# Kernel optimization log

Hardware: AMD Instinct MI355X
Metric: run time of the kernel (lower is better)

The kernel has to match this reference:

```python
import jax, jax.numpy as jnp
import numpy as np

BN_EPS = 1e-5


def conv_bn_relu(x, w, b, gamma, beta):
    # Conv2d(stride=2, padding=1) -> BatchNorm2d (training-mode batch stats) -> ReLU
    y = jax.lax.conv_general_dilated(
        x, w, window_strides=(2, 2), padding=((1, 1), (1, 1)),
        dimension_numbers=('NCHW', 'OIHW', 'NCHW')) + b[None, :, None, None]
    mu = y.mean(axis=(0, 2, 3))
    var = y.var(axis=(0, 2, 3))
    y = (y - mu[None, :, None, None]) * jax.lax.rsqrt(var + BN_EPS)[None, :, None, None]
    y = y * gamma[None, :, None, None] + beta[None, :, None, None]
    return jax.nn.relu(y)


def setup_inputs() -> dict:
    key = jax.random.key(0)
    ks = jax.random.split(key, 12)
    N, C, HW_IN = 32, 3, 64
    SD = 24           # stem_dim
    RQ = 128          # rnn_hidden_dim
    MD = 128          # module_dim
    FC = 1024         # classifier hidden
    NA = 2            # num answers
    D_PAIR = (SD + 2) * 2 + RQ  # 180
    s = 0.05
    return {
        'image':   jax.random.normal(ks[0], (N, C, HW_IN, HW_IN), jnp.float32),
        'ques':    jax.random.normal(ks[1], (N, RQ), jnp.float32),
        'conv1_w': jax.random.normal(ks[2], (SD, C, 3, 3), jnp.float32) * s,
        'conv1_b': jnp.zeros((SD,), jnp.float32),
        'bn1_g':   jnp.ones((SD,), jnp.float32),
        'bn1_b':   jnp.zeros((SD,), jnp.float32),
        'conv2_w': jax.random.normal(ks[3], (SD, SD, 3, 3), jnp.float32) * s,
        'conv2_b': jnp.zeros((SD,), jnp.float32),
        'bn2_g':   jnp.ones((SD,), jnp.float32),
        'bn2_b':   jnp.zeros((SD,), jnp.float32),
        'w_rel':   jax.random.normal(ks[4], (D_PAIR, MD), jnp.float32) * s,
        'b_rel':   jnp.zeros((MD,), jnp.float32),
        'w_fc1':   jax.random.normal(ks[5], (MD, FC), jnp.float32) * s,
        'b_fc1':   jnp.zeros((FC,), jnp.float32),
        'w_fc2':   jax.random.normal(ks[6], (FC, NA), jnp.float32) * s,
        'b_fc2':   jnp.zeros((NA,), jnp.float32),
    }


def reference(image, ques, conv1_w, conv1_b, bn1_g, bn1_b,
              conv2_w, conv2_b, bn2_g, bn2_b,
              w_rel, b_rel, w_fc1, b_fc1, w_fc2, b_fc2):
    f = conv_bn_relu(image, conv1_w, conv1_b, bn1_g, bn1_b)
    f = conv_bn_relu(f, conv2_w, conv2_b, bn2_g, bn2_b)
    N, F, H, W = f.shape
    HW = H * W
    flat = f.reshape(N, F, HW).transpose(0, 2, 1)      # (N, HW, F)

    # coordinate grid exactly as in the torch code (stacked over (W, H))
    xs = jnp.linspace(-1.0, 1.0, W)
    ys = jnp.linspace(-1.0, 1.0, H)
    xv = jnp.repeat(xs[:, None], H, axis=1)            # (W, H)
    yv = jnp.repeat(ys[None, :], W, axis=0)            # (W, H)
    coords = jnp.stack([xv, yv], axis=2).reshape(-1, 2)  # (HW, 2)

    fc = jnp.concatenate(
        [flat, jnp.broadcast_to(coords[None], (N, HW, 2))], axis=2)  # (N, HW, F+2)
    D = F + 2

    # relation layer is a single Linear over cat([x_i, x_j, ques]) followed by
    # a sum over ALL (HW)^2 pairs. Because the layer is linear, the pair sum
    # decomposes exactly:
    #   sum_{a,b} (fc[b] Wi + fc[a] Wj + q Wq + b_rel)
    # = HW * (sum_p fc[p]) (Wi + Wj) + HW^2 * (q Wq + b_rel)
    Wi, Wj, Wq = w_rel[:D], w_rel[D:2 * D], w_rel[2 * D:]
    s = fc.sum(axis=1)                                  # (N, D)
    hw = jnp.asarray(HW, fc.dtype)
    relations = hw * (s @ (Wi + Wj)) + (hw * hw) * (ques @ Wq + b_rel)  # (N, 128)

    # ---- classifier: Linear -> ReLU -> Linear ----
    h = jax.nn.relu(relations @ w_fc1 + b_fc1)
    out = h @ w_fc2 + b_fc2                             # (N, num_answers)
    return out
```

## Files before the change

### kernel.cpp

```cpp
#include <hip/hip_runtime.h>
#include <math.h>


#define N_BATCH 32
#define C_OUT 24
#define NBLK 192
#define MAGIC 0x13579BDFu
#define AGENT __HIP_MEMORY_SCOPE_AGENT
#define PITCH 40
#define NROWS 33
#define CHSZ (PITCH * NROWS)

__device__ __forceinline__ float aload(const float* p) {
  return __hip_atomic_load(p, __ATOMIC_RELAXED, AGENT);
}
__device__ __forceinline__ void astore(float* p, float v) {
  __hip_atomic_store(p, v, __ATOMIC_RELAXED, AGENT);
}
__device__ __forceinline__ void waitflag(const unsigned* f) {
  while (__hip_atomic_load(f, __ATOMIC_RELAXED, AGENT) != MAGIC)
    __builtin_amdgcn_s_sleep(1);
}

__global__ __launch_bounds__(1024) void fused_kernel(
    const float* __restrict__ img, const float* __restrict__ ques,
    const float* __restrict__ c1w, const float* __restrict__ c1b,
    const float* __restrict__ g1,  const float* __restrict__ bt1,
    const float* __restrict__ c2w, const float* __restrict__ c2b,
    const float* __restrict__ g2,  const float* __restrict__ bt2,
    const float* __restrict__ w_rel, const float* __restrict__ b_rel,
    const float* __restrict__ w_fc1, const float* __restrict__ b_fc1,
    const float* __restrict__ w_fc2, const float* __restrict__ b_fc2,
    float* __restrict__ out,
    unsigned* __restrict__ flags1, unsigned* __restrict__ flags2,
    unsigned* __restrict__ flags3,
    float* __restrict__ p1, float* __restrict__ p2,
    float* __restrict__ ssum) {
  const int t = threadIdx.x;
  const int bid = blockIdx.x;
  const int lane = t & 63, wid = t >> 6;
  const int n = bid & 31;
  const int r = bid >> 5;

  __shared__ unsigned short y1u[24 * CHSZ];
  __shared__ float red[5120];
  __shared__ float s_a[C_OUT], s_b[C_OUT];
  __shared__ float a2[4], b2[4];
  __shared__ float chS[16], chS2[16];
  __shared__ float qpart[1024];
  __shared__ float qfull[128];
  __shared__ float s_s[26];
  __shared__ float s_coef[128];
  __shared__ float s_h[1024];

  if (t < 24 * PITCH) {
    int ch = t / PITCH;
    y1u[ch * CHSZ + (t - ch * PITCH)] = 0;
  }
  if (t < 768)
    y1u[(t >> 5) * CHSZ + ((t & 31) + 1) * PITCH] = 0;

  {
    int oh = t >> 5, ow = t & 31;
    float win[27];
    #pragma unroll
    for (int ci = 0; ci < 3; ci++)
      #pragma unroll
      for (int kh = 0; kh < 3; kh++) {
        int ih = oh * 2 - 1 + kh;
        #pragma unroll
        for (int kw = 0; kw < 3; kw++) {
          int iw = ow * 2 - 1 + kw;
          win[ci * 9 + kh * 3 + kw] =
              (ih >= 0 && iw >= 0) ? img[(n * 3 + ci) * 4096 + ih * 64 + iw] : 0.f;
        }
      }
    #pragma unroll
    for (int co = 0; co < C_OUT; co++) {
      float acc = c1b[co];
      #pragma unroll
      for (int q = 0; q < 27; q++) acc += win[q] * c1w[co * 27 + q];
      unsigned bits = __float_as_uint(acc);
      unsigned rr = (bits + 0x7FFFu + ((bits >> 16) & 1u)) >> 16;
      y1u[co * CHSZ + (oh + 1) * PITCH + (ow + 1)] = (unsigned short)rr;
    }
  }
  __syncthreads();

  if (r == 0) {
    if (t < 768) {
      int ch = t >> 5, l = t & 31;
      float s = 0.f, s2 = 0.f;
      #pragma unroll
      for (int i = 0; i < 32; i++) {
        float x = __uint_as_float(
            (unsigned)y1u[ch * CHSZ + (i + 1) * PITCH + (l + 1)] << 16);
        s += x; s2 += x * x;
      }
      #pragma unroll
      for (int off = 16; off > 0; off >>= 1) {
        s += __shfl_down(s, off, 32);
        s2 += __shfl_down(s2, off, 32);
      }
      if (l == 0) {
        astore(&p1[ch * 32 + n], s);
        astore(&p1[768 + ch * 32 + n], s2);
      }
    }
    __syncthreads();
    if (t == 0)
      __hip_atomic_store(&flags1[n], MAGIC, __ATOMIC_RELEASE, AGENT);
  }

  if (t < 32) waitflag(&flags1[t]);
  __syncthreads();
  if (t < 768) {
    int ch = t >> 5, j = t & 31;
    float s = aload(&p1[ch * 32 + j]);
    float s2 = aload(&p1[768 + ch * 32 + j]);
    #pragma unroll
    for (int off = 16; off > 0; off >>= 1) {
      s += __shfl_down(s, off, 32);
      s2 += __shfl_down(s2, off, 32);
    }
    if (j == 0) {
      float mu = s * (1.f / 32768.f);
      float var = s2 * (1.f / 32768.f) - mu * mu;
      float a = rsqrtf(var + 1e-5f) * g1[ch];
      s_a[ch] = a;
      s_b[ch] = bt1[ch] - mu * a;
    }
  }
  __syncthreads();

  const int px = t & 255;
  const int slot = t >> 8;
  const int co2 = r * 4 + slot;
  float acc2;
  {
    const int o2h = px >> 4, o2w = px & 15;
    float accq[4] = {0.f, 0.f, 0.f, 0.f};
    const int ci0 = slot * 6;
    #pragma unroll
    for (int cc = 0; cc < 6; cc++) {
      const int ci = ci0 + cc;
      const float a1 = s_a[ci], b1 = s_b[ci];
      const unsigned* chp = (const unsigned*)(y1u + ci * CHSZ);
      #pragma unroll
      for (int kh = 0; kh < 3; kh++) {
        const int row = o2h * 2 + kh;
        const unsigned* pr = chp + row * (PITCH / 2);
        unsigned w0 = pr[o2w];
        unsigned w1 = pr[o2w + 1];
        float x0 = __uint_as_float(w0 << 16);
        float x1 = __uint_as_float(w0 & 0xffff0000u);
        float x2 = __uint_as_float(w1 << 16);
        x0 = fmaxf(fmaf(x0, a1, b1), 0.f);
        x1 = fmaxf(fmaf(x1, a1, b1), 0.f);
        x2 = fmaxf(fmaf(x2, a1, b1), 0.f);
        if (row == 0) { x0 = 0.f; x1 = 0.f; x2 = 0.f; }
        if (o2w == 0) x0 = 0.f;
        #pragma unroll
        for (int co = 0; co < 4; co++) {
          const float* wp = c2w + ((r * 4 + co) * C_OUT + ci) * 9 + kh * 3;
          accq[co] = fmaf(x0, wp[0], accq[co]);
          accq[co] = fmaf(x1, wp[1], accq[co]);
          accq[co] = fmaf(x2, wp[2], accq[co]);
        }
      }
    }
    #pragma unroll
    for (int q = 0; q < 4; q++) red[(slot * 256 + px) * 5 + q] = accq[q];
  }
  __syncthreads();
  {
    acc2 = c2b[co2];
    #pragma unroll
    for (int s = 0; s < 4; s++) acc2 += red[(s * 256 + px) * 5 + slot];
  }
  {
    float s = acc2, s2 = acc2 * acc2;
    #pragma unroll
    for (int off = 32; off > 0; off >>= 1) {
      s += __shfl_down(s, off, 64);
      s2 += __shfl_down(s2, off, 64);
    }
    if (lane == 0) { chS[slot * 4 + (wid & 3)] = s; chS2[slot * 4 + (wid & 3)] = s2; }
  }
  __syncthreads();
  if (t < 4) {
    float s = chS[t * 4] + chS[t * 4 + 1] + chS[t * 4 + 2] + chS[t * 4 + 3];
    float s2 = chS2[t * 4] + chS2[t * 4 + 1] + chS2[t * 4 + 2] + chS2[t * 4 + 3];
    astore(&p2[(r * 4 + t) * 32 + n], s);
    astore(&p2[768 + (r * 4 + t) * 32 + n], s2);
  }
  __syncthreads();
  if (t == 0)
    __hip_atomic_store(&flags2[bid], MAGIC, __ATOMIC_RELEASE, AGENT);

  if (r == 0) {
    {
      float pf = 0.f;
      #pragma unroll
      for (int i = 0; i < 4; i++) pf += w_fc1[(t + i * 1024) * 32];
      if (t < 208) pf += w_rel[t * 32];
      if (t < 64)  pf += w_fc2[t * 32];
      if (t < 32)  pf += b_fc1[t * 32];
      asm volatile("" :: "v"(pf));
    }
    {
      int m = t & 127, g = t >> 7;
      const float* qv = ques + n * 128;
      float q = 0.f;
      for (int k = g * 16; k < g * 16 + 16; k++)
        q += qv[k] * w_rel[(52 + k) * 128 + m];
      qpart[t] = q;
    }
    __syncthreads();
    if (t < 128) {
      float q = b_rel[t];
      #pragma unroll
      for (int g = 0; g < 8; g++) q += qpart[g * 128 + t];
      qfull[t] = 65536.f * q;
    }
  }

  if (t < 32) waitflag(&flags2[r * 32 + t]);
  __syncthreads();
  if (t < 128) {
    int c4 = t >> 5, j = t & 31;
    float s = aload(&p2[(r * 4 + c4) * 32 + j]);
    float s2 = aload(&p2[768 + (r * 4 + c4) * 32 + j]);
    #pragma unroll
    for (int off = 16; off > 0; off >>= 1) {
      s += __shfl_down(s, off, 32);
      s2 += __shfl_down(s2, off, 32);
    }
    if (j == 0) {
      float mu = s * (1.f / 8192.f);
      float var = s2 * (1.f / 8192.f) - mu * mu;
      float a = rsqrtf(var + 1e-5f) * g2[r * 4 + c4];
      a2[c4] = a;
      b2[c4] = bt2[r * 4 + c4] - mu * a;
    }
  }
  __syncthreads();

  {
    float v = acc2 * a2[slot] + b2[slot];
    v = v > 0.f ? v : 0.f;
    #pragma unroll
    for (int off = 32; off > 0; off >>= 1) v += __shfl_down(v, off, 64);
    if (lane == 0) chS[slot * 4 + (wid & 3)] = v;
  }
  __syncthreads();
  if (t < 4)
    astore(&ssum[n * C_OUT + r * 4 + t],
           chS[t * 4] + chS[t * 4 + 1] + chS[t * 4 + 2] + chS[t * 4 + 3]);
  __syncthreads();
  if (t == 0)
    __hip_atomic_store(&flags3[bid], MAGIC, __ATOMIC_RELEASE, AGENT);

  if (r != 0) return;

  if (t >= 1 && t < 6) waitflag(&flags3[t * 32 + n]);
  __syncthreads();
  if (t < C_OUT) s_s[t] = aload(&ssum[n * C_OUT + t]);
  if (t == 24 || t == 25) {
    float cs = 0.f;
    for (int i = 0; i < 16; i++) cs += -1.f + 2.f * (float)i / 15.f;
    s_s[t] = 16.f * cs;
  }
  __syncthreads();

  {
    int col = t & 127, g = t >> 7;
    float p = 0.f;
    #pragma unroll
    for (int dd = 0; dd < 4; dd++) {
      int d = g + dd * 8;
      if (d < 26)
        p += s_s[d] * (w_rel[d * 128 + col] + w_rel[(26 + d) * 128 + col]);
    }
    qpart[t] = p;
  }
  __syncthreads();
  if (t < 128) {
    float sterm = 0.f;
    #pragma unroll
    for (int g = 0; g < 8; g++) sterm += qpart[g * 128 + t];
    s_coef[t] = qfull[t] + 256.f * sterm;
  }
  __syncthreads();

  {
    const int cg = t & 255, mg = t >> 8;
    const float4* wp = (const float4*)(w_fc1) + mg * 32 * 256 + cg;
    float4 acc = make_float4(0.f, 0.f, 0.f, 0.f);
    #pragma unroll 8
    for (int k = 0; k < 32; k++) {
      float c = s_coef[mg * 32 + k];
      float4 w = wp[k * 256];
      acc.x += c * w.x; acc.y += c * w.y; acc.z += c * w.z; acc.w += c * w.w;
    }
    red[cg * 17 + mg * 4 + 0] = acc.x;
    red[cg * 17 + mg * 4 + 1] = acc.y;
    red[cg * 17 + mg * 4 + 2] = acc.z;
    red[cg * 17 + mg * 4 + 3] = acc.w;
  }
  __syncthreads();
  {
    float h = b_fc1[t];
    #pragma unroll
    for (int mg = 0; mg < 4; mg++) h += red[(t >> 2) * 17 + mg * 4 + (t & 3)];
    s_h[t] = h > 0.f ? h : 0.f;
  }
  __syncthreads();

  {
    float hv = s_h[t];
    float a0 = hv * w_fc2[2 * t], a1 = hv * w_fc2[2 * t + 1];
    #pragma unroll
    for (int off = 32; off > 0; off >>= 1) {
      a0 += __shfl_down(a0, off, 64);
      a1 += __shfl_down(a1, off, 64);
    }
    if (lane == 0) { chS[wid] = a0; chS2[wid] = a1; }
  }
  __syncthreads();
  if (t == 0) {
    float a0 = 0.f, a1 = 0.f;
    #pragma unroll
    for (int i = 0; i < 16; i++) { a0 += chS[i]; a1 += chS2[i]; }
    out[n * 2 + 0] = a0 + b_fc2[0];
    out[n * 2 + 1] = a1 + b_fc2[1];
  }
}

extern "C" void kernel_launch(void* const* d_in, const int* in_sizes, int n_in,
                              void* d_out, int out_size, void* d_ws, size_t ws_size,
                              hipStream_t stream) {
  const float* image   = (const float*)d_in[0];
  const float* ques    = (const float*)d_in[1];
  const float* conv1_w = (const float*)d_in[2];
  const float* conv1_b = (const float*)d_in[3];
  const float* bn1_g   = (const float*)d_in[4];
  const float* bn1_b   = (const float*)d_in[5];
  const float* conv2_w = (const float*)d_in[6];
  const float* conv2_b = (const float*)d_in[7];
  const float* bn2_g   = (const float*)d_in[8];
  const float* bn2_b   = (const float*)d_in[9];
  const float* w_rel   = (const float*)d_in[10];
  const float* b_rel   = (const float*)d_in[11];
  const float* w_fc1   = (const float*)d_in[12];
  const float* b_fc1   = (const float*)d_in[13];
  const float* w_fc2   = (const float*)d_in[14];
  const float* b_fc2   = (const float*)d_in[15];
  float* out = (float*)d_out;

  unsigned* flags1 = (unsigned*)d_ws;
  unsigned* flags2 = flags1 + 32;
  unsigned* flags3 = flags2 + 192;
  float* p1   = (float*)d_ws + 416;
  float* p2   = p1 + 1536;
  float* ssum = p2 + 1536;

  fused_kernel<<<NBLK, 1024, 0, stream>>>(
      image, ques, conv1_w, conv1_b, bn1_g, bn1_b, conv2_w, conv2_b,
      bn2_g, bn2_b, w_rel, b_rel, w_fc1, b_fc1, w_fc2, b_fc2,
      out, flags1, flags2, flags3, p1, p2, ssum);
}
```

Measured before the change: 120.7 us.

## Split classifier FC1/FC2 across all six row-blocks per sample

Before, only the r==0 block of each sample computed the 128x1024 FC1 and FC2 tail while the other five blocks exited. Now every block computes the relation coefficients and its own slice of about 43 float4 column groups of FC1. It reduces FC2 partials for that slice and hands them to r==0 through a new flag and partial buffer. Weight prefetch is also spread across all blocks earlier. This cuts the serial tail on one block per sample, at the cost of an extra cross-block handoff and redundant qfull/coef computation in every block.

```diff
diff --git a/kernel.cpp b/kernel.cpp
--- a/kernel.cpp
+++ b/kernel.cpp
@@ -33,17 +33,20 @@
     const float* __restrict__ w_fc2, const float* __restrict__ b_fc2,
     float* __restrict__ out,
     unsigned* __restrict__ flags1, unsigned* __restrict__ flags2,
-    unsigned* __restrict__ flags3,
+    unsigned* __restrict__ flags3, unsigned* __restrict__ flags4,
     float* __restrict__ p1, float* __restrict__ p2,
-    float* __restrict__ ssum) {
+    float* __restrict__ ssum, float* __restrict__ pairs) {
   const int t = threadIdx.x;
   const int bid = blockIdx.x;
   const int lane = t & 63, wid = t >> 6;
   const int n = bid & 31;
   const int r = bid >> 5;
 
+  const int g0 = r * 43 - (r == 5 ? 1 : 0);
+  const int gcnt = (r < 4) ? 43 : 42;
+
   __shared__ unsigned short y1u[24 * CHSZ];
-  __shared__ float red[5120];
+  __align__(16) __shared__ float red[5120];
   __shared__ float s_a[C_OUT], s_b[C_OUT];
   __shared__ float a2[4], b2[4];
   __shared__ float chS[16], chS2[16];
@@ -51,7 +54,6 @@
   __shared__ float qfull[128];
   __shared__ float s_s[26];
   __shared__ float s_coef[128];
-  __shared__ float s_h[1024];
 
   if (t < 24 * PITCH) {
     int ch = t / PITCH;
@@ -110,6 +112,20 @@
     __syncthreads();
     if (t == 0)
       __hip_atomic_store(&flags1[n], MAGIC, __ATOMIC_RELEASE, AGENT);
+  }
+
+  {
+    float pf = 0.f;
+    {
+      int row = t >> 3, l = t & 7;
+      int col = g0 * 4 + l * 32;
+      col = col < 1024 ? col : 1023;
+      pf += w_fc1[row * 1024 + col];
+    }
+    if (t < 720) pf += w_rel[t * 32];
+    if (t < 64)  pf += w_fc2[t * 32];
+    if (t < 32)  pf += b_fc1[t * 32];
+    asm volatile("" :: "v"(pf));
   }
 
   if (t < 32) waitflag(&flags1[t]);
@@ -198,31 +214,20 @@
   if (t == 0)
     __hip_atomic_store(&flags2[bid], MAGIC, __ATOMIC_RELEASE, AGENT);
 
-  if (r == 0) {
-    {
-      float pf = 0.f;
-      #pragma unroll
-      for (int i = 0; i < 4; i++) pf += w_fc1[(t + i * 1024) * 32];
-      if (t < 208) pf += w_rel[t * 32];
-      if (t < 64)  pf += w_fc2[t * 32];
-      if (t < 32)  pf += b_fc1[t * 32];
-      asm volatile("" :: "v"(pf));
-    }
-    {
-      int m = t & 127, g = t >> 7;
-      const float* qv = ques + n * 128;
-      float q = 0.f;
-      for (int k = g * 16; k < g * 16 + 16; k++)
-        q += qv[k] * w_rel[(52 + k) * 128 + m];
-      qpart[t] = q;
-    }
-    __syncthreads();
-    if (t < 128) {
-      float q = b_rel[t];
-      #pragma unroll
-      for (int g = 0; g < 8; g++) q += qpart[g * 128 + t];
-      qfull[t] = 65536.f * q;
-    }
+  {
+    int m = t & 127, g = t >> 7;
+    const float* qv = ques + n * 128;
+    float q = 0.f;
+    for (int k = g * 16; k < g * 16 + 16; k++)
+      q += qv[k] * w_rel[(52 + k) * 128 + m];
+    qpart[t] = q;
+  }
+  __syncthreads();
+  if (t < 128) {
+    float q = b_rel[t];
+    #pragma unroll
+    for (int g = 0; g < 8; g++) q += qpart[g * 128 + t];
+    qfull[t] = 65536.f * q;
   }
 
   if (t < 32) waitflag(&flags2[r * 32 + t]);
@@ -261,9 +266,7 @@
   if (t == 0)
     __hip_atomic_store(&flags3[bid], MAGIC, __ATOMIC_RELEASE, AGENT);
 
-  if (r != 0) return;
-
-  if (t >= 1 && t < 6) waitflag(&flags3[t * 32 + n]);
+  if (t < 6 && t != r) waitflag(&flags3[t * 32 + n]);
   __syncthreads();
   if (t < C_OUT) s_s[t] = aload(&ssum[n * C_OUT + t]);
   if (t == 24 || t == 25) {
@@ -294,32 +297,33 @@
   __syncthreads();
 
   {
-    const int cg = t & 255, mg = t >> 8;
-    const float4* wp = (const float4*)(w_fc1) + mg * 32 * 256 + cg;
-    float4 acc = make_float4(0.f, 0.f, 0.f, 0.f);
-    #pragma unroll 8
-    for (int k = 0; k < 32; k++) {
-      float c = s_coef[mg * 32 + k];
-      float4 w = wp[k * 256];
-      acc.x += c * w.x; acc.y += c * w.y; acc.z += c * w.z; acc.w += c * w.w;
-    }
-    red[cg * 17 + mg * 4 + 0] = acc.x;
-    red[cg * 17 + mg * 4 + 1] = acc.y;
-    red[cg * 17 + mg * 4 + 2] = acc.z;
-    red[cg * 17 + mg * 4 + 3] = acc.w;
-  }
-  __syncthreads();
-  {
-    float h = b_fc1[t];
-    #pragma unroll
-    for (int mg = 0; mg < 4; mg++) h += red[(t >> 2) * 17 + mg * 4 + (t & 3)];
-    s_h[t] = h > 0.f ? h : 0.f;
-  }
-  __syncthreads();
-
-  {
-    float hv = s_h[t];
-    float a0 = hv * w_fc2[2 * t], a1 = hv * w_fc2[2 * t + 1];
+    const int gi = lane, mseg = wid;
+    if (gi < gcnt) {
+      const float4* wp = (const float4*)w_fc1 + (g0 + gi);
+      float4 acc = make_float4(0.f, 0.f, 0.f, 0.f);
+      #pragma unroll
+      for (int k = 0; k < 8; k++) {
+        int m = mseg * 8 + k;
+        float c = s_coef[m];
+        float4 w = wp[m * 256];
+        acc.x += c * w.x; acc.y += c * w.y; acc.z += c * w.z; acc.w += c * w.w;
+      }
+      ((float4*)red)[mseg * 43 + gi] = acc;
+    }
+  }
+  __syncthreads();
+  float a0 = 0.f, a1 = 0.f;
+  if (t < gcnt * 4) {
+    const int gcol = g0 * 4 + t;
+    float h = b_fc1[gcol];
+    #pragma unroll
+    for (int mseg = 0; mseg < 16; mseg++) h += red[mseg * 172 + t];
+    h = h > 0.f ? h : 0.f;
+    a0 = h * w_fc2[2 * gcol];
+    a1 = h * w_fc2[2 * gcol + 1];
+  }
+  __syncthreads();
+  {
     #pragma unroll
     for (int off = 32; off > 0; off >>= 1) {
       a0 += __shfl_down(a0, off, 64);
@@ -329,11 +333,30 @@
   }
   __syncthreads();
   if (t == 0) {
-    float a0 = 0.f, a1 = 0.f;
-    #pragma unroll
-    for (int i = 0; i < 16; i++) { a0 += chS[i]; a1 += chS2[i]; }
-    out[n * 2 + 0] = a0 + b_fc2[0];
-    out[n * 2 + 1] = a1 + b_fc2[1];
+    float b0 = 0.f, b1v = 0.f;
+    #pragma unroll
+    for (int i = 0; i < 16; i++) { b0 += chS[i]; b1v += chS2[i]; }
+    if (r != 0) {
+      astore(&pairs[n * 12 + r * 2 + 0], b0);
+      astore(&pairs[n * 12 + r * 2 + 1], b1v);
+      __hip_atomic_store(&flags4[bid], MAGIC, __ATOMIC_RELEASE, AGENT);
+    } else {
+      chS[0] = b0; chS2[0] = b1v;
+    }
+  }
+  if (r != 0) return;
+
+  if (t >= 1 && t < 6) waitflag(&flags4[t * 32 + n]);
+  __syncthreads();
+  if (t == 0) {
+    float b0 = chS[0], b1v = chS2[0];
+    #pragma unroll
+    for (int i = 1; i < 6; i++) {
+      b0 += aload(&pairs[n * 12 + i * 2 + 0]);
+      b1v += aload(&pairs[n * 12 + i * 2 + 1]);
+    }
+    out[n * 2 + 0] = b0 + b_fc2[0];
+    out[n * 2 + 1] = b1v + b_fc2[1];
   }
 }
 
@@ -361,12 +384,14 @@
   unsigned* flags1 = (unsigned*)d_ws;
   unsigned* flags2 = flags1 + 32;
   unsigned* flags3 = flags2 + 192;
-  float* p1   = (float*)d_ws + 416;
-  float* p2   = p1 + 1536;
-  float* ssum = p2 + 1536;
+  unsigned* flags4 = flags3 + 192;
+  float* p1    = (float*)d_ws + 608;
+  float* p2    = p1 + 1536;
+  float* ssum  = p2 + 1536;
+  float* pairs = ssum + 768;
 
   fused_kernel<<<NBLK, 1024, 0, stream>>>(
       image, ques, conv1_w, conv1_b, bn1_g, bn1_b, conv2_w, conv2_b,
       bn2_g, bn2_b, w_rel, b_rel, w_fc1, b_fc1, w_fc2, b_fc2,
-      out, flags1, flags2, flags3, p1, p2, ssum);
-}
+      out, flags1, flags2, flags3, flags4, p1, p2, ssum, pairs);
+}
```

Result: slower. 124.4 us (+3.0%).

## Collapse to one block per image, dropping cross-block output-channel split and third barrier

Applied to the files above, without the earlier changes.

Launches 32 blocks (one per batch image) instead of 192, so each block computes all 24 conv2 output channels itself rather than splitting channels across 6 blocks. This removes the in-block partial-sum reduction through shared memory, the third global flag barrier and the ssum exchange. It also reuses the y1 shared buffer for the FC reduction and widens the L2 prefetch of w_rel. The cost is that conv2 work per block grows sixfold and only 32 CUs are used, so the critical path per block lengthens.

```diff
diff --git a/kernel.cpp b/kernel.cpp
--- a/kernel.cpp
+++ b/kernel.cpp
@@ -2,14 +2,12 @@
 #include <math.h>
 
 
-#define N_BATCH 32
-#define C_OUT 24
-#define NBLK 192
 #define MAGIC 0x13579BDFu
 #define AGENT __HIP_MEMORY_SCOPE_AGENT
 #define PITCH 40
 #define NROWS 33
 #define CHSZ (PITCH * NROWS)
+#define C_OUT 24
 
 __device__ __forceinline__ float aload(const float* p) {
   return __hip_atomic_load(p, __ATOMIC_RELAXED, AGENT);
@@ -33,25 +31,21 @@
     const float* __restrict__ w_fc2, const float* __restrict__ b_fc2,
     float* __restrict__ out,
     unsigned* __restrict__ flags1, unsigned* __restrict__ flags2,
-    unsigned* __restrict__ flags3,
-    float* __restrict__ p1, float* __restrict__ p2,
-    float* __restrict__ ssum) {
+    float* __restrict__ p1, float* __restrict__ p2) {
   const int t = threadIdx.x;
-  const int bid = blockIdx.x;
+  const int n = blockIdx.x;
   const int lane = t & 63, wid = t >> 6;
-  const int n = bid & 31;
-  const int r = bid >> 5;
-
-  __shared__ unsigned short y1u[24 * CHSZ];
-  __shared__ float red[5120];
+
+  __shared__ __align__(16) unsigned short y1u[24 * CHSZ];
   __shared__ float s_a[C_OUT], s_b[C_OUT];
-  __shared__ float a2[4], b2[4];
-  __shared__ float chS[16], chS2[16];
+  __shared__ float s_a2[C_OUT], s_b2[C_OUT];
+  __shared__ float chS[96], chS2[96];
   __shared__ float qpart[1024];
   __shared__ float qfull[128];
   __shared__ float s_s[26];
   __shared__ float s_coef[128];
-  __shared__ float s_h[1024];
+
+  float* red = (float*)y1u;
 
   if (t < 24 * PITCH) {
     int ch = t / PITCH;
@@ -87,29 +81,37 @@
   }
   __syncthreads();
 
-  if (r == 0) {
-    if (t < 768) {
-      int ch = t >> 5, l = t & 31;
-      float s = 0.f, s2 = 0.f;
-      #pragma unroll
-      for (int i = 0; i < 32; i++) {
-        float x = __uint_as_float(
-            (unsigned)y1u[ch * CHSZ + (i + 1) * PITCH + (l + 1)] << 16);
-        s += x; s2 += x * x;
-      }
-      #pragma unroll
-      for (int off = 16; off > 0; off >>= 1) {
-        s += __shfl_down(s, off, 32);
-        s2 += __shfl_down(s2, off, 32);
-      }
-      if (l == 0) {
-        astore(&p1[ch * 32 + n], s);
-        astore(&p1[768 + ch * 32 + n], s2);
-      }
-    }
-    __syncthreads();
-    if (t == 0)
-      __hip_atomic_store(&flags1[n], MAGIC, __ATOMIC_RELEASE, AGENT);
+  if (t < 768) {
+    int ch = t >> 5, l = t & 31;
+    float s = 0.f, s2 = 0.f;
+    #pragma unroll
+    for (int i = 0; i < 32; i++) {
+      float x = __uint_as_float(
+          (unsigned)y1u[ch * CHSZ + (i + 1) * PITCH + (l + 1)] << 16);
+      s += x; s2 += x * x;
+    }
+    #pragma unroll
+    for (int off = 16; off > 0; off >>= 1) {
+      s += __shfl_down(s, off, 32);
+      s2 += __shfl_down(s2, off, 32);
+    }
+    if (l == 0) {
+      astore(&p1[ch * 32 + n], s);
+      astore(&p1[768 + ch * 32 + n], s2);
+    }
+  }
+  __syncthreads();
+  if (t == 0)
+    __hip_atomic_store(&flags1[n], MAGIC, __ATOMIC_RELEASE, AGENT);
+
+  {
+    float pf = 0.f;
+    #pragma unroll
+    for (int i = 0; i < 4; i++) pf += w_fc1[(t + i * 1024) * 32];
+    if (t < 720) pf += w_rel[t * 32];
+    if (t < 64)  pf += w_fc2[t * 32];
+    if (t < 32)  pf += b_fc1[t * 32];
+    asm volatile("" :: "v"(pf));
   }
 
   if (t < 32) waitflag(&flags1[t]);
@@ -134,16 +136,14 @@
   __syncthreads();
 
   const int px = t & 255;
-  const int slot = t >> 8;
-  const int co2 = r * 4 + slot;
-  float acc2;
+  const int sgrp = t >> 8;
+  const int cb = sgrp * 6;
+  float acc[6];
   {
     const int o2h = px >> 4, o2w = px & 15;
-    float accq[4] = {0.f, 0.f, 0.f, 0.f};
-    const int ci0 = slot * 6;
-    #pragma unroll
-    for (int cc = 0; cc < 6; cc++) {
-      const int ci = ci0 + cc;
+    #pragma unroll
+    for (int j = 0; j < 6; j++) acc[j] = c2b[cb + j];
+    for (int ci = 0; ci < 24; ci++) {
       const float a1 = s_a[ci], b1 = s_b[ci];
       const unsigned* chp = (const unsigned*)(y1u + ci * CHSZ);
       #pragma unroll
@@ -161,76 +161,62 @@
         if (row == 0) { x0 = 0.f; x1 = 0.f; x2 = 0.f; }
         if (o2w == 0) x0 = 0.f;
         #pragma unroll
-        for (int co = 0; co < 4; co++) {
-          const float* wp = c2w + ((r * 4 + co) * C_OUT + ci) * 9 + kh * 3;
-          accq[co] = fmaf(x0, wp[0], accq[co]);
-          accq[co] = fmaf(x1, wp[1], accq[co]);
-          accq[co] = fmaf(x2, wp[2], accq[co]);
+        for (int j = 0; j < 6; j++) {
+          const float* wp = c2w + ((cb + j) * C_OUT + ci) * 9 + kh * 3;
+          acc[j] = fmaf(x0, wp[0], fmaf(x1, wp[1], fmaf(x2, wp[2], acc[j])));
         }
       }
     }
-    #pragma unroll
-    for (int q = 0; q < 4; q++) red[(slot * 256 + px) * 5 + q] = accq[q];
-  }
-  __syncthreads();
-  {
-    acc2 = c2b[co2];
-    #pragma unroll
-    for (int s = 0; s < 4; s++) acc2 += red[(s * 256 + px) * 5 + slot];
-  }
-  {
-    float s = acc2, s2 = acc2 * acc2;
-    #pragma unroll
-    for (int off = 32; off > 0; off >>= 1) {
-      s += __shfl_down(s, off, 64);
-      s2 += __shfl_down(s2, off, 64);
-    }
-    if (lane == 0) { chS[slot * 4 + (wid & 3)] = s; chS2[slot * 4 + (wid & 3)] = s2; }
-  }
-  __syncthreads();
-  if (t < 4) {
+  }
+
+  {
+    #pragma unroll
+    for (int j = 0; j < 6; j++) {
+      float s = acc[j], s2 = acc[j] * acc[j];
+      #pragma unroll
+      for (int off = 32; off > 0; off >>= 1) {
+        s += __shfl_down(s, off, 64);
+        s2 += __shfl_down(s2, off, 64);
+      }
+      if (lane == 0) {
+        chS[(cb + j) * 4 + (wid & 3)] = s;
+        chS2[(cb + j) * 4 + (wid & 3)] = s2;
+      }
+    }
+  }
+  __syncthreads();
+  if (t < C_OUT) {
     float s = chS[t * 4] + chS[t * 4 + 1] + chS[t * 4 + 2] + chS[t * 4 + 3];
     float s2 = chS2[t * 4] + chS2[t * 4 + 1] + chS2[t * 4 + 2] + chS2[t * 4 + 3];
-    astore(&p2[(r * 4 + t) * 32 + n], s);
-    astore(&p2[768 + (r * 4 + t) * 32 + n], s2);
+    astore(&p2[t * 32 + n], s);
+    astore(&p2[768 + t * 32 + n], s2);
   }
   __syncthreads();
   if (t == 0)
-    __hip_atomic_store(&flags2[bid], MAGIC, __ATOMIC_RELEASE, AGENT);
-
-  if (r == 0) {
-    {
-      float pf = 0.f;
-      #pragma unroll
-      for (int i = 0; i < 4; i++) pf += w_fc1[(t + i * 1024) * 32];
-      if (t < 208) pf += w_rel[t * 32];
-      if (t < 64)  pf += w_fc2[t * 32];
-      if (t < 32)  pf += b_fc1[t * 32];
-      asm volatile("" :: "v"(pf));
-    }
-    {
-      int m = t & 127, g = t >> 7;
-      const float* qv = ques + n * 128;
-      float q = 0.f;
-      for (int k = g * 16; k < g * 16 + 16; k++)
-        q += qv[k] * w_rel[(52 + k) * 128 + m];
-      qpart[t] = q;
-    }
-    __syncthreads();
-    if (t < 128) {
-      float q = b_rel[t];
-      #pragma unroll
-      for (int g = 0; g < 8; g++) q += qpart[g * 128 + t];
-      qfull[t] = 65536.f * q;
-    }
-  }
-
-  if (t < 32) waitflag(&flags2[r * 32 + t]);
+    __hip_atomic_store(&flags2[n], MAGIC, __ATOMIC_RELEASE, AGENT);
+
+  {
+    int m = t & 127, g = t >> 7;
+    const float* qv = ques + n * 128;
+    float q = 0.f;
+    for (int k = g * 16; k < g * 16 + 16; k++)
+      q += qv[k] * w_rel[(52 + k) * 128 + m];
+    qpart[t] = q;
+  }
   __syncthreads();
   if (t < 128) {
-    int c4 = t >> 5, j = t & 31;
-    float s = aload(&p2[(r * 4 + c4) * 32 + j]);
-    float s2 = aload(&p2[768 + (r * 4 + c4) * 32 + j]);
+    float q = b_rel[t];
+    #pragma unroll
+    for (int g = 0; g < 8; g++) q += qpart[g * 128 + t];
+    qfull[t] = 65536.f * q;
+  }
+
+  if (t < 32) waitflag(&flags2[t]);
+  __syncthreads();
+  if (t < 768) {
+    int ch = t >> 5, j = t & 31;
+    float s = aload(&p2[ch * 32 + j]);
+    float s2 = aload(&p2[768 + ch * 32 + j]);
     #pragma unroll
     for (int off = 16; off > 0; off >>= 1) {
       s += __shfl_down(s, off, 32);
@@ -239,33 +225,26 @@
     if (j == 0) {
       float mu = s * (1.f / 8192.f);
       float var = s2 * (1.f / 8192.f) - mu * mu;
-      float a = rsqrtf(var + 1e-5f) * g2[r * 4 + c4];
-      a2[c4] = a;
-      b2[c4] = bt2[r * 4 + c4] - mu * a;
-    }
-  }
-  __syncthreads();
-
-  {
-    float v = acc2 * a2[slot] + b2[slot];
-    v = v > 0.f ? v : 0.f;
-    #pragma unroll
-    for (int off = 32; off > 0; off >>= 1) v += __shfl_down(v, off, 64);
-    if (lane == 0) chS[slot * 4 + (wid & 3)] = v;
-  }
-  __syncthreads();
-  if (t < 4)
-    astore(&ssum[n * C_OUT + r * 4 + t],
-           chS[t * 4] + chS[t * 4 + 1] + chS[t * 4 + 2] + chS[t * 4 + 3]);
-  __syncthreads();
-  if (t == 0)
-    __hip_atomic_store(&flags3[bid], MAGIC, __ATOMIC_RELEASE, AGENT);
-
-  if (r != 0) return;
-
-  if (t >= 1 && t < 6) waitflag(&flags3[t * 32 + n]);
-  __syncthreads();
-  if (t < C_OUT) s_s[t] = aload(&ssum[n * C_OUT + t]);
+      float a = rsqrtf(var + 1e-5f) * g2[ch];
+      s_a2[ch] = a;
+      s_b2[ch] = bt2[ch] - mu * a;
+    }
+  }
+  __syncthreads();
+
+  {
+    #pragma unroll
+    for (int j = 0; j < 6; j++) {
+      float v = acc[j] * s_a2[cb + j] + s_b2[cb + j];
+      v = v > 0.f ? v : 0.f;
+      #pragma unroll
+      for (int off = 32; off > 0; off >>= 1) v += __shfl_down(v, off, 64);
+      if (lane == 0) chS[(cb + j) * 4 + (wid & 3)] = v;
+    }
+  }
+  __syncthreads();
+  if (t < C_OUT)
+    s_s[t] = chS[t * 4] + chS[t * 4 + 1] + chS[t * 4 + 2] + chS[t * 4 + 3];
   if (t == 24 || t == 25) {
     float cs = 0.f;
     for (int i = 0; i < 16; i++) cs += -1.f + 2.f * (float)i / 15.f;
@@ -296,44 +275,44 @@
   {
     const int cg = t & 255, mg = t >> 8;
     const float4* wp = (const float4*)(w_fc1) + mg * 32 * 256 + cg;
-    float4 acc = make_float4(0.f, 0.f, 0.f, 0.f);
+    float4 a4 = make_float4(0.f, 0.f, 0.f, 0.f);
     #pragma unroll 8
     for (int k = 0; k < 32; k++) {
       float c = s_coef[mg * 32 + k];
       float4 w = wp[k * 256];
-      acc.x += c * w.x; acc.y += c * w.y; acc.z += c * w.z; acc.w += c * w.w;
-    }
-    red[cg * 17 + mg * 4 + 0] = acc.x;
-    red[cg * 17 + mg * 4 + 1] = acc.y;
-    red[cg * 17 + mg * 4 + 2] = acc.z;
-    red[cg * 17 + mg * 4 + 3] = acc.w;
-  }
-  __syncthreads();
+      a4.x += c * w.x; a4.y += c * w.y; a4.z += c * w.z; a4.w += c * w.w;
+    }
+    red[cg * 17 + mg * 4 + 0] = a4.x;
+    red[cg * 17 + mg * 4 + 1] = a4.y;
+    red[cg * 17 + mg * 4 + 2] = a4.z;
+    red[cg * 17 + mg * 4 + 3] = a4.w;
+  }
+  __syncthreads();
+  float a0, a1v;
   {
     float h = b_fc1[t];
     #pragma unroll
     for (int mg = 0; mg < 4; mg++) h += red[(t >> 2) * 17 + mg * 4 + (t & 3)];
-    s_h[t] = h > 0.f ? h : 0.f;
-  }
-  __syncthreads();
-
-  {
-    float hv = s_h[t];
-    float a0 = hv * w_fc2[2 * t], a1 = hv * w_fc2[2 * t + 1];
+    h = h > 0.f ? h : 0.f;
+    a0 = h * w_fc2[2 * t];
+    a1v = h * w_fc2[2 * t + 1];
+  }
+  __syncthreads();
+  {
     #pragma unroll
     for (int off = 32; off > 0; off >>= 1) {
       a0 += __shfl_down(a0, off, 64);
-      a1 += __shfl_down(a1, off, 64);
-    }
-    if (lane == 0) { chS[wid] = a0; chS2[wid] = a1; }
+      a1v += __shfl_down(a1v, off, 64);
+    }
+    if (lane == 0) { chS[wid] = a0; chS2[wid] = a1v; }
   }
   __syncthreads();
   if (t == 0) {
-    float a0 = 0.f, a1 = 0.f;
-    #pragma unroll
-    for (int i = 0; i < 16; i++) { a0 += chS[i]; a1 += chS2[i]; }
-    out[n * 2 + 0] = a0 + b_fc2[0];
-    out[n * 2 + 1] = a1 + b_fc2[1];
+    float b0 = 0.f, b1 = 0.f;
+    #pragma unroll
+    for (int i = 0; i < 16; i++) { b0 += chS[i]; b1 += chS2[i]; }
+    out[n * 2 + 0] = b0 + b_fc2[0];
+    out[n * 2 + 1] = b1 + b_fc2[1];
   }
 }
 
@@ -360,13 +339,11 @@
 
   unsigned* flags1 = (unsigned*)d_ws;
   unsigned* flags2 = flags1 + 32;
-  unsigned* flags3 = flags2 + 192;
-  float* p1   = (float*)d_ws + 416;
-  float* p2   = p1 + 1536;
-  float* ssum = p2 + 1536;
-
-  fused_kernel<<<NBLK, 1024, 0, stream>>>(
+  float* p1 = (float*)d_ws + 64;
+  float* p2 = p1 + 1536;
+
+  fused_kernel<<<32, 1024, 0, stream>>>(
       image, ques, conv1_w, conv1_b, bn1_g, bn1_b, conv2_w, conv2_b,
       bn2_g, bn2_b, w_rel, b_rel, w_fc1, b_fc1, w_fc2, b_fc2,
-      out, flags1, flags2, flags3, p1, p2, ssum);
-}
+      out, flags1, flags2, p1, p2);
+}
```

After: 151.5 us. +25.5%, slower.
